# Kernel optimization log

Measured on AMD Instinct MI355X. Metric: run time of the kernel, lower is better.

## Reference

```python
import jax, jax.numpy as jnp
import numpy as np

EMBED_DIM = 1024
NUM_HEADS = 16
HEAD_DIM = EMBED_DIM // NUM_HEADS
B, S = 8, 1024


def setup_inputs() -> dict:
    key = jax.random.key(0)
    k1, k2, k3, k4, k5 = jax.random.split(key, 5)
    scale_in = 1.0 / np.sqrt(EMBED_DIM)
    return {
        "qkv": jax.random.normal(k1, (B, S, EMBED_DIM), dtype=jnp.float32),
        "w_in": jax.random.normal(k2, (3 * EMBED_DIM, EMBED_DIM), dtype=jnp.float32) * scale_in,
        "b_in": jax.random.normal(k3, (3 * EMBED_DIM,), dtype=jnp.float32) * 0.01,
        "w_out": jax.random.normal(k4, (EMBED_DIM, EMBED_DIM), dtype=jnp.float32) * scale_in,
        "b_out": jax.random.normal(k5, (EMBED_DIM,), dtype=jnp.float32) * 0.01,
    }


def reference(qkv, w_in, b_in, w_out, b_out):
    # in_proj: [B,S,E] -> [B,S,3E]  (torch Linear: x @ W.T + b)
    proj = qkv @ w_in.T + b_in
    q, k, v = jnp.split(proj, 3, axis=2)
    # split heads: [B,S,E] -> [B,S,H,D]
    def heads(t):
        return t.reshape(B, S, NUM_HEADS, HEAD_DIM)
    q, k, v = heads(q), heads(k), heads(v)
    # scaled dot-product attention per head; scale = sqrt(head_dim)
    scores = jnp.einsum("bqhd,bkhd->bhqk", q, k) / jnp.sqrt(jnp.float32(HEAD_DIM))
    attn = jax.nn.softmax(scores, axis=-1)
    out = jnp.einsum("bhqk,bkhd->bqhd", attn, v)  # [B,S,H,D]
    out = out.reshape(B, S, EMBED_DIM)  # concat heads along feature dim
    return out @ w_out.T + b_out
```

## Files before the change

kernel.cpp:

```cpp
#include <hip/hip_runtime.h>

typedef _Float16 f16;
typedef _Float16 f16x4 __attribute__((ext_vector_type(4)));
typedef _Float16 f16x8 __attribute__((ext_vector_type(8)));
typedef float f32x4 __attribute__((ext_vector_type(4)));
typedef float f32x16 __attribute__((ext_vector_type(16)));
typedef unsigned u32x4 __attribute__((ext_vector_type(4)));

#define DEVINL __device__ __forceinline__
#define VMCNT(n) asm volatile("s_waitcnt vmcnt(" #n ")" ::: "memory")
#define SCHEDBAR() __builtin_amdgcn_sched_barrier(0)

DEVINL void gload16(const void* g, void* l) {
    __builtin_amdgcn_global_load_lds(
        (const __attribute__((address_space(1))) unsigned int*)g,
        (__attribute__((address_space(3))) unsigned int*)l, 16, 0, 0);
}

DEVINL unsigned pk2(float a, float b) {
    auto v = __builtin_amdgcn_cvt_pkrtz(a, b);
    return __builtin_bit_cast(unsigned, v);
}

__global__ __launch_bounds__(256) void cvt_kernel(const float* __restrict__ in,
                                                  f16* __restrict__ out, int n4) {
    int i = blockIdx.x * 256 + threadIdx.x;
    int st = gridDim.x * 256;
    for (; i < n4; i += st) {
        float4 v = reinterpret_cast<const float4*>(in)[i];
        f16x4 o = {(f16)v.x, (f16)v.y, (f16)v.z, (f16)v.w};
        reinterpret_cast<f16x4*>(out)[i] = o;
    }
}

__global__ __launch_bounds__(256) void gemm_in(const f16* __restrict__ A,
                                               const f16* __restrict__ Bm,
                                               const float* __restrict__ bias,
                                               f16* __restrict__ Qw, f16* __restrict__ Kw,
                                               f16* __restrict__ Vtw) {
    constexpr int K = 1024, NT = K / 32;
    __shared__ f16 As[2][128 * 32];
    __shared__ f16 Bs[2][128 * 32];
    const int t = threadIdx.x;
    const int wave = t >> 6, lane = t & 63, lr = lane & 15, lg = lane >> 4;
    const int wr = wave >> 1, wc = wave & 1;
    const int wg = blockIdx.x;
    const int swz = (wg & 7) * 192 + (wg >> 3);
    const int m0 = (swz / 24) * 128, n0 = (swz % 24) * 128;

    const f16* Ag = A + (m0 + (t >> 2)) * K + (t & 3) * 8;
    const f16* Bg = Bm + (n0 + (t >> 2)) * K + (t & 3) * 8;

    f32x4 acc[4][4] = {};

    auto stage = [&](int buf, int kt) {
        const f16* a = Ag + kt * 32;
        const f16* b = Bg + kt * 32;
        f16* al = &As[buf][t * 8];
        f16* bl = &Bs[buf][t * 8];
        gload16(a, al);
        gload16(a + 64 * K, al + 64 * 32);
        gload16(b, bl);
        gload16(b + 64 * K, bl + 64 * 32);
    };

    stage(0, 0);
    __syncthreads();
    int cur = 0;
    for (int kt = 0; kt < NT; ++kt) {
        if (kt + 1 < NT) stage(cur ^ 1, kt + 1);
        const f16* as = &As[cur][0];
        const f16* bs = &Bs[cur][0];
        f16x8 af[4], bf[4];
#pragma unroll
        for (int i = 0; i < 4; ++i)
            af[i] = *(const f16x8*)&as[(wr * 64 + i * 16 + lr) * 32 + lg * 8];
#pragma unroll
        for (int i = 0; i < 4; ++i)
            bf[i] = *(const f16x8*)&bs[(wc * 64 + i * 16 + lr) * 32 + lg * 8];
#pragma unroll
        for (int i = 0; i < 4; ++i)
#pragma unroll
            for (int j = 0; j < 4; ++j)
                acc[i][j] = __builtin_amdgcn_mfma_f32_16x16x32_f16(af[i], bf[j], acc[i][j], 0, 0, 0);
        __syncthreads();
        cur ^= 1;
    }

    const float SCQ = 0.18033688011112042f;
#pragma unroll
    for (int nf = 0; nf < 4; ++nf) {
        int n = n0 + wc * 64 + nf * 16 + lr;
        float bv = bias[n];
        int part = n >> 10, e = n & 1023, hh = e >> 6, dd = e & 63;
#pragma unroll
        for (int mf = 0; mf < 4; ++mf) {
            int m = m0 + wr * 64 + mf * 16 + lg * 4;
            int bb = m >> 10, ss = m & 1023;
            if (part == 0) {
                f16* dst = Qw + ((bb * 16 + hh) * 1024 + ss) * 64 + dd;
#pragma unroll
                for (int r = 0; r < 4; ++r) dst[r * 64] = (f16)((acc[mf][nf][r] + bv) * SCQ);
            } else if (part == 1) {
                f16* dst = Kw + ((bb * 16 + hh) * 1024 + ss) * 64 + dd;
#pragma unroll
                for (int r = 0; r < 4; ++r) dst[r * 64] = (f16)(acc[mf][nf][r] + bv);
            } else {
                f16x4 pkv;
#pragma unroll
                for (int r = 0; r < 4; ++r) pkv[r] = (f16)(acc[mf][nf][r] + bv);
                *(f16x4*)(Vtw + ((bb * 16 + hh) * 64 + dd) * 1024 + ss) = pkv;
            }
        }
    }
}

__global__ __launch_bounds__(256) void gemm_out(const f16* __restrict__ A,
                                                const f16* __restrict__ Bm,
                                                const float* __restrict__ bias,
                                                float* __restrict__ Cout) {
    constexpr int K = 1024, NT = K / 32;
    __shared__ f16 As[2][128 * 32];
    __shared__ f16 Bs[2][128 * 32];
    const int t = threadIdx.x;
    const int wave = t >> 6, lane = t & 63, lr = lane & 15, lg = lane >> 4;
    const int wr = wave >> 1, wc = wave & 1;
    const int wg = blockIdx.x;
    const int swz = (wg & 7) * 64 + (wg >> 3);
    const int m0 = (swz / 8) * 128, n0 = (swz % 8) * 128;

    const f16* Ag = A + (m0 + (t >> 2)) * K + (t & 3) * 8;
    const f16* Bg = Bm + (n0 + (t >> 2)) * K + (t & 3) * 8;

    f32x4 acc[4][4] = {};

    auto stage = [&](int buf, int kt) {
        const f16* a = Ag + kt * 32;
        const f16* b = Bg + kt * 32;
        f16* al = &As[buf][t * 8];
        f16* bl = &Bs[buf][t * 8];
        gload16(a, al);
        gload16(a + 64 * K, al + 64 * 32);
        gload16(b, bl);
        gload16(b + 64 * K, bl + 64 * 32);
    };

    stage(0, 0);
    __syncthreads();
    int cur = 0;
    for (int kt = 0; kt < NT; ++kt) {
        if (kt + 1 < NT) stage(cur ^ 1, kt + 1);
        const f16* as = &As[cur][0];
        const f16* bs = &Bs[cur][0];
        f16x8 af[4], bf[4];
#pragma unroll
        for (int i = 0; i < 4; ++i)
            af[i] = *(const f16x8*)&as[(wr * 64 + i * 16 + lr) * 32 + lg * 8];
#pragma unroll
        for (int i = 0; i < 4; ++i)
            bf[i] = *(const f16x8*)&bs[(wc * 64 + i * 16 + lr) * 32 + lg * 8];
#pragma unroll
        for (int i = 0; i < 4; ++i)
#pragma unroll
            for (int j = 0; j < 4; ++j)
                acc[i][j] = __builtin_amdgcn_mfma_f32_16x16x32_f16(af[i], bf[j], acc[i][j], 0, 0, 0);
        __syncthreads();
        cur ^= 1;
    }
#pragma unroll
    for (int nf = 0; nf < 4; ++nf) {
        int n = n0 + wc * 64 + nf * 16 + lr;
        float bv = bias[n];
#pragma unroll
        for (int mf = 0; mf < 4; ++mf) {
            int m = m0 + wr * 64 + mf * 16 + lg * 4;
#pragma unroll
            for (int r = 0; r < 4; ++r) Cout[(m + r) * 1024 + n] = acc[mf][nf][r] + bv;
        }
    }
}

__global__ __launch_bounds__(256) void attn_kernel(const f16* __restrict__ Qw,
                                                   const f16* __restrict__ Kw,
                                                   const f16* __restrict__ Vtw,
                                                   f16* __restrict__ AO) {
    __shared__ char LDSb[65536];
    const int t = threadIdx.x, wave = t >> 6, lane = t & 63;
    const int ql = lane & 31, hi = lane >> 5;
    const int wg = blockIdx.x;
    const int gid = (wg & 7) * 128 + (wg >> 3);
    const int qt = gid & 7, h = (gid >> 3) & 15, b = gid >> 7;
    const f16* Qp = Qw + (b * 16 + h) * 1024 * 64;
    const f16* Kp = Kw + (b * 16 + h) * 1024 * 64;
    const f16* Vp = Vtw + (b * 16 + h) * 64 * 1024;
    const int q0 = qt * 128 + wave * 32;

    f16x8 qb[4];
#pragma unroll
    for (int s = 0; s < 4; ++s)
        qb[s] = *(const f16x8*)&Qp[(q0 + ql) * 64 + s * 16 + hi * 8];

    const int srow0 = t >> 3;
    const int sw = (t & 7) << 4;
    auto stage_kv = [&](int slot, int kv) {
#pragma unroll
        for (int c = 0; c < 2; ++c) {
            int row = c * 32 + srow0;
            int gwb = sw ^ ((row & 7) << 4);
            gload16((const char*)(Kp + (kv + row) * 64) + gwb,
                    LDSb + slot * 8192 + c * 4096 + t * 16);
            gload16((const char*)(Vp + row * 1024 + kv) + gwb,
                    LDSb + 32768 + slot * 8192 + c * 4096 + t * 16);
        }
    };

    f32x16 o0 = 0.f, o1 = 0.f;
    float mraw = -1e30f, lsum = 0.f;

    stage_kv(0, 0);
    stage_kv(1, 64);
    stage_kv(2, 128);
    VMCNT(8);

    for (int kv = 0; kv < 16; ++kv) {
        __builtin_amdgcn_s_barrier();
        SCHEDBAR();
        if (kv + 3 < 16) stage_kv((kv + 3) & 3, (kv + 3) * 64);
        const char* Kb = LDSb + (kv & 3) * 8192;
        const char* Vb = LDSb + 32768 + (kv & 3) * 8192;

        f32x16 st0, st1;
        __builtin_amdgcn_s_setprio(1);
#pragma unroll
        for (int s = 0; s < 4; ++s) {
            int byt = (s * 32 + hi * 16) ^ ((ql & 7) << 4);
            f16x8 k0 = *(const f16x8*)(Kb + ql * 128 + byt);
            f16x8 k1 = *(const f16x8*)(Kb + (32 + ql) * 128 + byt);
            if (s == 0) {
                st0 = __builtin_amdgcn_mfma_f32_32x32x16_f16(k0, qb[0], (f32x16)0.f, 0, 0, 0);
                st1 = __builtin_amdgcn_mfma_f32_32x32x16_f16(k1, qb[0], (f32x16)0.f, 0, 0, 0);
            } else {
                st0 = __builtin_amdgcn_mfma_f32_32x32x16_f16(k0, qb[s], st0, 0, 0, 0);
                st1 = __builtin_amdgcn_mfma_f32_32x32x16_f16(k1, qb[s], st1, 0, 0, 0);
            }
        }
        __builtin_amdgcn_s_setprio(0);

        float a[16];
#pragma unroll
        for (int r = 0; r < 16; ++r) a[r] = fmaxf(st0[r], st1[r]);
#pragma unroll
        for (int s = 8; s >= 1; s >>= 1)
#pragma unroll
            for (int r = 0; r < 16; ++r)
                if (r < s) a[r] = fmaxf(a[r], a[r + s]);
        float mx = fmaxf(a[0], __shfl_xor(a[0], 32, 64));

        if (__all(mx <= mraw + 8.f)) {
#pragma unroll
            for (int r = 0; r < 16; ++r) st0[r] = exp2f(st0[r] - mraw);
#pragma unroll
            for (int r = 0; r < 16; ++r) st1[r] = exp2f(st1[r] - mraw);
            float sa[16];
#pragma unroll
            for (int r = 0; r < 16; ++r) sa[r] = st0[r] + st1[r];
#pragma unroll
            for (int s = 8; s >= 1; s >>= 1)
#pragma unroll
                for (int r = 0; r < 16; ++r)
                    if (r < s) sa[r] += sa[r + s];
            lsum += sa[0] + __shfl_xor(sa[0], 32, 64);
        } else {
            float mn = fmaxf(mraw, mx);
            float al = exp2f(mraw - mn);
            mraw = mn;
#pragma unroll
            for (int r = 0; r < 16; ++r) st0[r] = exp2f(st0[r] - mn);
#pragma unroll
            for (int r = 0; r < 16; ++r) st1[r] = exp2f(st1[r] - mn);
            float sa[16];
#pragma unroll
            for (int r = 0; r < 16; ++r) sa[r] = st0[r] + st1[r];
#pragma unroll
            for (int s = 8; s >= 1; s >>= 1)
#pragma unroll
                for (int r = 0; r < 16; ++r)
                    if (r < s) sa[r] += sa[r + s];
            lsum = lsum * al + sa[0] + __shfl_xor(sa[0], 32, 64);
            o0 *= al;
            o1 *= al;
        }

#pragma unroll
        for (int s = 0; s < 4; ++s) {
            const int s1 = s & 1;
            float p0, p1, p2, p3, p4, p5, p6, p7;
            if (s < 2) {
                p0 = st0[8 * s1 + 0]; p1 = st0[8 * s1 + 1]; p2 = st0[8 * s1 + 2]; p3 = st0[8 * s1 + 3];
                p4 = st0[8 * s1 + 4]; p5 = st0[8 * s1 + 5]; p6 = st0[8 * s1 + 6]; p7 = st0[8 * s1 + 7];
            } else {
                p0 = st1[8 * s1 + 0]; p1 = st1[8 * s1 + 1]; p2 = st1[8 * s1 + 2]; p3 = st1[8 * s1 + 3];
                p4 = st1[8 * s1 + 4]; p5 = st1[8 * s1 + 5]; p6 = st1[8 * s1 + 6]; p7 = st1[8 * s1 + 7];
            }
            unsigned c0 = pk2(p0, p1), c1 = pk2(p2, p3);
            unsigned c2 = pk2(p4, p5), c3 = pk2(p6, p7);
            unsigned y0 = __shfl_xor(hi ? c0 : c2, 32, 64);
            unsigned y1 = __shfl_xor(hi ? c1 : c3, 32, 64);
            unsigned w0 = hi ? y0 : c0;
            unsigned w1 = hi ? y1 : c1;
            unsigned w2 = hi ? c2 : y0;
            unsigned w3 = hi ? c3 : y1;
            u32x4 pw = {w0, w1, w2, w3};
            f16x8 pf = __builtin_bit_cast(f16x8, pw);
            __builtin_amdgcn_s_setprio(1);
#pragma unroll
            for (int db = 0; db < 2; ++db) {
                int row = db * 32 + ql;
                int byt = (s * 32 + hi * 16) ^ ((row & 7) << 4);
                f16x8 vf = *(const f16x8*)(Vb + row * 128 + byt);
                if (db == 0)
                    o0 = __builtin_amdgcn_mfma_f32_32x32x16_f16(vf, pf, o0, 0, 0, 0);
                else
                    o1 = __builtin_amdgcn_mfma_f32_32x32x16_f16(vf, pf, o1, 0, 0, 0);
            }
            __builtin_amdgcn_s_setprio(0);
        }
        if (kv <= 12) VMCNT(8);
        else if (kv == 13) VMCNT(4);
        else if (kv == 14) VMCNT(0);
        SCHEDBAR();
    }

    SCHEDBAR();
    float inv = 1.0f / lsum;
    char* obase = LDSb + wave * 4096;
#pragma unroll
    for (int db = 0; db < 2; ++db)
#pragma unroll
        for (int r = 0; r < 16; ++r) {
            int d = db * 32 + (r & 3) + 8 * (r >> 2) + 4 * hi;
            float v = (db == 0 ? o0[r] : o1[r]) * inv;
            *(f16*)(obase + ql * 128 + ((2 * d) ^ ((ql & 7) << 4))) = (f16)v;
        }
    __syncthreads();
    const int rl = lane >> 1, c4 = (lane & 1) * 4;
#pragma unroll
    for (int i = 0; i < 4; ++i) {
        f16x8 ov = *(const f16x8*)(obase + rl * 128 + (((c4 + i) * 16) ^ ((rl & 7) << 4)));
        *(f16x8*)&AO[(b * 1024 + q0 + rl) * 1024 + h * 64 + (c4 + i) * 8] = ov;
    }
}

extern "C" void kernel_launch(void* const* d_in, const int* in_sizes, int n_in,
                              void* d_out, int out_size, void* d_ws, size_t ws_size,
                              hipStream_t stream) {
    const float* qkv = (const float*)d_in[0];
    const float* w_in = (const float*)d_in[1];
    const float* b_in = (const float*)d_in[2];
    const float* w_out = (const float*)d_in[3];
    const float* b_out = (const float*)d_in[4];
    float* out = (float*)d_out;

    f16* Xh = (f16*)d_ws;
    f16* Wih = Xh + 8388608;
    f16* Woh = Wih + 3145728;
    f16* Qw = Woh + 1048576;
    f16* Kw = Qw + 8388608;
    f16* Vtw = Kw + 8388608;
    f16* AO = Xh;

    cvt_kernel<<<2048, 256, 0, stream>>>(qkv, Xh, 8388608 / 4);
    cvt_kernel<<<1024, 256, 0, stream>>>(w_in, Wih, 3145728 / 4);
    cvt_kernel<<<512, 256, 0, stream>>>(w_out, Woh, 1048576 / 4);

    gemm_in<<<1536, 256, 0, stream>>>(Xh, Wih, b_in, Qw, Kw, Vtw);
    attn_kernel<<<1024, 256, 0, stream>>>(Qw, Kw, Vtw, AO);
    gemm_out<<<512, 256, 0, stream>>>(AO, Woh, b_out, out);
}
```

Baseline: 300.3 us.

## Fuse fp16 conversions, retile input GEMM to 128x256 with swizzled LDS, shrink attention buffers

```diff
diff --git a/kernel.cpp b/kernel.cpp
--- a/kernel.cpp
+++ b/kernel.cpp
@@ -22,80 +22,128 @@
     return __builtin_bit_cast(unsigned, v);
 }
 
-__global__ __launch_bounds__(256) void cvt_kernel(const float* __restrict__ in,
-                                                  f16* __restrict__ out, int n4) {
+__global__ __launch_bounds__(256) void cvt_all(const float* __restrict__ a,
+                                               const float* __restrict__ b,
+                                               const float* __restrict__ c,
+                                               f16* __restrict__ oa, f16* __restrict__ ob,
+                                               f16* __restrict__ oc) {
     int i = blockIdx.x * 256 + threadIdx.x;
     int st = gridDim.x * 256;
-    for (; i < n4; i += st) {
-        float4 v = reinterpret_cast<const float4*>(in)[i];
+    for (; i < 3145728; i += st) {
+        const float4* src;
+        f16* dst;
+        int j;
+        if (i < 2097152) { src = (const float4*)a; dst = oa; j = i; }
+        else if (i < 2883584) { src = (const float4*)b; dst = ob; j = i - 2097152; }
+        else { src = (const float4*)c; dst = oc; j = i - 2883584; }
+        float4 v = src[j];
         f16x4 o = {(f16)v.x, (f16)v.y, (f16)v.z, (f16)v.w};
-        reinterpret_cast<f16x4*>(out)[i] = o;
-    }
-}
-
-__global__ __launch_bounds__(256) void gemm_in(const f16* __restrict__ A,
+        reinterpret_cast<f16x4*>(dst)[j] = o;
+    }
+}
+
+__global__ __launch_bounds__(512) void gemm_in(const f16* __restrict__ A,
                                                const f16* __restrict__ Bm,
                                                const float* __restrict__ bias,
                                                f16* __restrict__ Qw, f16* __restrict__ Kw,
                                                f16* __restrict__ Vtw) {
-    constexpr int K = 1024, NT = K / 32;
-    __shared__ f16 As[2][128 * 32];
-    __shared__ f16 Bs[2][128 * 32];
-    const int t = threadIdx.x;
-    const int wave = t >> 6, lane = t & 63, lr = lane & 15, lg = lane >> 4;
-    const int wr = wave >> 1, wc = wave & 1;
+    __shared__ __align__(16) char SM[2][49152];
+    const int t = threadIdx.x, lane = t & 63, w = t >> 6;
+    const int lr = lane & 15, lg = lane >> 4;
+    const int wm = w >> 2, wn = w & 3;
     const int wg = blockIdx.x;
-    const int swz = (wg & 7) * 192 + (wg >> 3);
-    const int m0 = (swz / 24) * 128, n0 = (swz % 24) * 128;
-
-    const f16* Ag = A + (m0 + (t >> 2)) * K + (t & 3) * 8;
-    const f16* Bg = Bm + (n0 + (t >> 2)) * K + (t & 3) * 8;
+    const int swz = (wg & 7) * 96 + (wg >> 3);
+    const int m0 = (swz / 12) * 128, n0 = (swz % 12) * 256;
+
+    const int srow = t >> 3, scw = (t & 7) << 4;
+    auto stage = [&](int buf, int kt) {
+#pragma unroll
+        for (int c = 0; c < 2; ++c) {
+            int row = c * 64 + srow;
+            gload16((const char*)(A + (m0 + row) * 1024 + kt * 64) + (scw ^ ((row & 7) << 4)),
+                    &SM[buf][c * 8192 + t * 16]);
+        }
+#pragma unroll
+        for (int c = 0; c < 4; ++c) {
+            int row = c * 64 + srow;
+            gload16((const char*)(Bm + (n0 + row) * 1024 + kt * 64) + (scw ^ ((row & 7) << 4)),
+                    &SM[buf][16384 + c * 8192 + t * 16]);
+        }
+    };
+
+    int offA[4][2], offB[4][2];
+#pragma unroll
+    for (int mf = 0; mf < 4; ++mf) {
+        int row = wm * 64 + mf * 16 + lr;
+#pragma unroll
+        for (int ks = 0; ks < 2; ++ks)
+            offA[mf][ks] = row * 128 + ((ks * 64 + lg * 16) ^ ((lr & 7) << 4));
+    }
+#pragma unroll
+    for (int nf = 0; nf < 4; ++nf) {
+        int row = wn * 64 + nf * 16 + lr;
+#pragma unroll
+        for (int ks = 0; ks < 2; ++ks)
+            offB[nf][ks] = 16384 + row * 128 + ((ks * 64 + lg * 16) ^ ((lr & 7) << 4));
+    }
 
     f32x4 acc[4][4] = {};
 
-    auto stage = [&](int buf, int kt) {
-        const f16* a = Ag + kt * 32;
-        const f16* b = Bg + kt * 32;
-        f16* al = &As[buf][t * 8];
-        f16* bl = &Bs[buf][t * 8];
-        gload16(a, al);
-        gload16(a + 64 * K, al + 64 * 32);
-        gload16(b, bl);
-        gload16(b + 64 * K, bl + 64 * 32);
-    };
-
     stage(0, 0);
-    __syncthreads();
-    int cur = 0;
-    for (int kt = 0; kt < NT; ++kt) {
-        if (kt + 1 < NT) stage(cur ^ 1, kt + 1);
-        const f16* as = &As[cur][0];
-        const f16* bs = &Bs[cur][0];
-        f16x8 af[4], bf[4];
-#pragma unroll
-        for (int i = 0; i < 4; ++i)
-            af[i] = *(const f16x8*)&as[(wr * 64 + i * 16 + lr) * 32 + lg * 8];
-#pragma unroll
-        for (int i = 0; i < 4; ++i)
-            bf[i] = *(const f16x8*)&bs[(wc * 64 + i * 16 + lr) * 32 + lg * 8];
-#pragma unroll
-        for (int i = 0; i < 4; ++i)
-#pragma unroll
-            for (int j = 0; j < 4; ++j)
-                acc[i][j] = __builtin_amdgcn_mfma_f32_16x16x32_f16(af[i], bf[j], acc[i][j], 0, 0, 0);
-        __syncthreads();
-        cur ^= 1;
-    }
+    VMCNT(0);
+    __builtin_amdgcn_s_barrier();
+    for (int kt = 0; kt < 16; ++kt) {
+        SCHEDBAR();
+        const int cur = kt & 1;
+        if (kt < 15) stage(cur ^ 1, kt + 1);
+        const char* base = &SM[cur][0];
+        f16x8 af[4][2], bf[4][2];
+#pragma unroll
+        for (int mf = 0; mf < 4; ++mf)
+#pragma unroll
+            for (int ks = 0; ks < 2; ++ks) af[mf][ks] = *(const f16x8*)(base + offA[mf][ks]);
+#pragma unroll
+        for (int nf = 0; nf < 2; ++nf)
+#pragma unroll
+            for (int ks = 0; ks < 2; ++ks) bf[nf][ks] = *(const f16x8*)(base + offB[nf][ks]);
+        __builtin_amdgcn_s_setprio(1);
+#pragma unroll
+        for (int ks = 0; ks < 2; ++ks)
+#pragma unroll
+            for (int mf = 0; mf < 4; ++mf)
+#pragma unroll
+                for (int nf = 0; nf < 2; ++nf)
+                    acc[mf][nf] = __builtin_amdgcn_mfma_f32_16x16x32_f16(af[mf][ks], bf[nf][ks],
+                                                                         acc[mf][nf], 0, 0, 0);
+        __builtin_amdgcn_s_setprio(0);
+#pragma unroll
+        for (int nf = 2; nf < 4; ++nf)
+#pragma unroll
+            for (int ks = 0; ks < 2; ++ks) bf[nf][ks] = *(const f16x8*)(base + offB[nf][ks]);
+        __builtin_amdgcn_s_setprio(1);
+#pragma unroll
+        for (int ks = 0; ks < 2; ++ks)
+#pragma unroll
+            for (int mf = 0; mf < 4; ++mf)
+#pragma unroll
+                for (int nf = 2; nf < 4; ++nf)
+                    acc[mf][nf] = __builtin_amdgcn_mfma_f32_16x16x32_f16(af[mf][ks], bf[nf][ks],
+                                                                         acc[mf][nf], 0, 0, 0);
+        __builtin_amdgcn_s_setprio(0);
+        if (kt < 15) VMCNT(0);
+        __builtin_amdgcn_s_barrier();
+    }
+    SCHEDBAR();
 
     const float SCQ = 0.18033688011112042f;
 #pragma unroll
     for (int nf = 0; nf < 4; ++nf) {
-        int n = n0 + wc * 64 + nf * 16 + lr;
+        int n = n0 + wn * 64 + nf * 16 + lr;
         float bv = bias[n];
         int part = n >> 10, e = n & 1023, hh = e >> 6, dd = e & 63;
 #pragma unroll
         for (int mf = 0; mf < 4; ++mf) {
-            int m = m0 + wr * 64 + mf * 16 + lg * 4;
+            int m = m0 + wm * 64 + mf * 16 + lg * 4;
             int bb = m >> 10, ss = m & 1023;
             if (part == 0) {
                 f16* dst = Qw + ((bb * 16 + hh) * 1024 + ss) * 64 + dd;
@@ -184,7 +232,7 @@
                                                    const f16* __restrict__ Kw,
                                                    const f16* __restrict__ Vtw,
                                                    f16* __restrict__ AO) {
-    __shared__ char LDSb[65536];
+    __shared__ char LDSb[49152];
     const int t = threadIdx.x, wave = t >> 6, lane = t & 63;
     const int ql = lane & 31, hi = lane >> 5;
     const int wg = blockIdx.x;
@@ -210,7 +258,7 @@
             gload16((const char*)(Kp + (kv + row) * 64) + gwb,
                     LDSb + slot * 8192 + c * 4096 + t * 16);
             gload16((const char*)(Vp + row * 1024 + kv) + gwb,
-                    LDSb + 32768 + slot * 8192 + c * 4096 + t * 16);
+                    LDSb + 24576 + slot * 8192 + c * 4096 + t * 16);
         }
     };
 
@@ -219,15 +267,15 @@
 
     stage_kv(0, 0);
     stage_kv(1, 64);
-    stage_kv(2, 128);
-    VMCNT(8);
-
+    VMCNT(4);
+
+    int cs = 0, ps = 2;
     for (int kv = 0; kv < 16; ++kv) {
         __builtin_amdgcn_s_barrier();
         SCHEDBAR();
-        if (kv + 3 < 16) stage_kv((kv + 3) & 3, (kv + 3) * 64);
-        const char* Kb = LDSb + (kv & 3) * 8192;
-        const char* Vb = LDSb + 32768 + (kv & 3) * 8192;
+        if (kv + 2 < 16) stage_kv(ps, (kv + 2) * 64);
+        const char* Kb = LDSb + cs * 8192;
+        const char* Vb = LDSb + 24576 + cs * 8192;
 
         f32x16 st0, st1;
         __builtin_amdgcn_s_setprio(1);
@@ -325,15 +373,16 @@
             }
             __builtin_amdgcn_s_setprio(0);
         }
-        if (kv <= 12) VMCNT(8);
-        else if (kv == 13) VMCNT(4);
+        if (kv <= 13) VMCNT(4);
         else if (kv == 14) VMCNT(0);
         SCHEDBAR();
+        cs = (cs == 2) ? 0 : cs + 1;
+        ps = (ps == 2) ? 0 : ps + 1;
     }
 
     SCHEDBAR();
     float inv = 1.0f / lsum;
-    char* obase = LDSb + wave * 4096;
+    char* obase = LDSb + 8192 + wave * 4096;
 #pragma unroll
     for (int db = 0; db < 2; ++db)
 #pragma unroll
@@ -369,11 +418,8 @@
     f16* Vtw = Kw + 8388608;
     f16* AO = Xh;
 
-    cvt_kernel<<<2048, 256, 0, stream>>>(qkv, Xh, 8388608 / 4);
-    cvt_kernel<<<1024, 256, 0, stream>>>(w_in, Wih, 3145728 / 4);
-    cvt_kernel<<<512, 256, 0, stream>>>(w_out, Woh, 1048576 / 4);
-
-    gemm_in<<<1536, 256, 0, stream>>>(Xh, Wih, b_in, Qw, Kw, Vtw);
+    cvt_all<<<2048, 256, 0, stream>>>(qkv, w_in, w_out, Xh, Wih, Woh);
+    gemm_in<<<768, 512, 0, stream>>>(Xh, Wih, b_in, Qw, Kw, Vtw);
     attn_kernel<<<1024, 256, 0, stream>>>(Qw, Kw, Vtw, AO);
     gemm_out<<<512, 256, 0, stream>>>(AO, Woh, b_out, out);
 }
```

Measured after the change: 291.2 us. 3.0% less time.
